# Kernel optimization log

Hardware: AMD Instinct MI355X
Metric: run time of the kernel (lower is better)

## Reference

```python
import jax, jax.numpy as jnp
import numpy as np

K = 5          # receptive field
N_IN = 4       # inputs per LUT node
DEPTH = 2      # tree depth -> layer widths [16, 4, 1]


def lut_nodes(s, lut):
    """Differentiable DWN LUT nodes.
    s:   [P, C, N, n] selected inputs in [0,1]
    lut: [C, N, 2**n] raw LUT weights (sigmoid applied -> entries in (0,1))
    out[p,c,m] = sum_a sigmoid(lut[c,m,a]) * prod_j s_j^{bit_j(a)} (1-s_j)^{1-bit_j(a)}
    Evaluated by contracting one address bit at a time (bit j=0 most significant).
    """
    n = s.shape[-1]
    C, N = lut.shape[0], lut.shape[1]
    t = jax.nn.sigmoid(lut).reshape((C, N) + (2,) * n)  # [C,N,2,...,2]
    for j in reversed(range(n)):
        xb = s[..., j].reshape(s.shape[:-1] + (1,) * j)  # [P,C,N,1*j]
        t = t[..., 0] * (1.0 - xb) + t[..., 1] * xb
    return t  # [P, C, N]


def extract_patches(x):
    """nn.Unfold(kernel=K, stride=1, pad=0): x [B,Cin,H,W] -> [B*P, Cin*K*K]."""
    B, Cin, H, W = x.shape
    Hp, Wp = H - K + 1, W - K + 1
    cols = jnp.stack([x[:, :, i:i + Hp, j:j + Wp]
                      for i in range(K) for j in range(K)], axis=2)  # [B,Cin,K*K,Hp,Wp]
    patches = cols.reshape(B, Cin * K * K, Hp * Wp)
    return patches.transpose(0, 2, 1).reshape(B * Hp * Wp, Cin * K * K), (B, Hp, Wp)


def setup_inputs() -> dict:
    key = jax.random.key(0)
    ks = jax.random.split(key, 7)
    C = 64
    return {
        "x": jax.random.uniform(ks[0], (32, 1, 32, 32), dtype=jnp.float32),
        "lut0": jax.random.normal(ks[1], (C, 16, 16), dtype=jnp.float32),
        "lut1": jax.random.normal(ks[2], (C, 4, 16), dtype=jnp.float32),
        "lut2": jax.random.normal(ks[3], (C, 1, 16), dtype=jnp.float32),
        "idx0": jax.random.randint(ks[4], (C, 16, N_IN), 0, 25, dtype=jnp.int32),
        "idx1": jax.random.randint(ks[5], (C, 4, N_IN), 0, 16, dtype=jnp.int32),
        "idx2": jax.random.randint(ks[6], (C, 1, N_IN), 0, 4, dtype=jnp.int32),
    }


def reference(x, lut0, lut1, lut2, idx0, idx1, idx2):
    patches, (B, Hp, Wp) = extract_patches(x)          # [P, 25]
    C = lut0.shape[0]
    # layer 0: gather raw patch features per channel/node
    s0 = patches[:, idx0]                              # [P, C, 16, 4]
    h0 = lut_nodes(s0, lut0)                           # [P, C, 16]
    # layer 1: per-channel gather from previous layer
    s1 = jnp.take_along_axis(h0[:, :, None, :], idx1[None], axis=-1)  # [P, C, 4, 4]
    h1 = lut_nodes(s1, lut1)                           # [P, C, 4]
    # layer 2 (root)
    s2 = jnp.take_along_axis(h1[:, :, None, :], idx2[None], axis=-1)  # [P, C, 1, 4]
    h2 = lut_nodes(s2, lut2)[..., 0]                   # [P, C]
    out = h2.reshape(B, Hp * Wp, C).transpose(0, 2, 1).reshape(B, C, Hp, Wp)
    return out
```

## Files before the change

kernel.cpp:

```cpp
#include <hip/hip_runtime.h>
#include <math.h>

#define KK 5
#define WPOUT 28
#define PPI 784
#define NCH 64
#define NPAIR 12544
#define THREADS 512
#define NNODE 21

typedef float f32x32 __attribute__((ext_vector_type(32)));
typedef float f32x16 __attribute__((ext_vector_type(16)));
typedef _Float16 h2  __attribute__((ext_vector_type(2)));

static __device__ __forceinline__ h2 u2h(unsigned u) { return __builtin_bit_cast(h2, u); }
static __device__ __forceinline__ unsigned h2u(h2 h) { return __builtin_bit_cast(unsigned, h); }
static __device__ __forceinline__ unsigned f2u(float f) { return __builtin_bit_cast(unsigned, f); }
static __device__ __forceinline__ float u2f(unsigned u) { return __builtin_bit_cast(float, u); }

static __device__ __forceinline__ unsigned packpair(float a, float b) {
    const auto pk = __builtin_amdgcn_cvt_pkrtz(a, b);
    return __builtin_bit_cast(unsigned, pk);
}

template <int ODD>
static __device__ __forceinline__ unsigned pkfma_splat(unsigned s, unsigned d, unsigned e) {
    unsigned r;
    if constexpr (ODD)
        asm("v_pk_fma_f16 %0, %1, %2, %3 op_sel:[0,1,1] op_sel_hi:[1,1,1]"
            : "=v"(r) : "v"(s), "v"(d), "v"(e));
    else
        asm("v_pk_fma_f16 %0, %1, %2, %3 op_sel:[0,0,0] op_sel_hi:[1,0,0]"
            : "=v"(r) : "v"(s), "v"(d), "v"(e));
    return r;
}

static __device__ __forceinline__ unsigned node_pair(uint4 E, uint4 D,
                                                     unsigned s0, unsigned s1,
                                                     unsigned s2, unsigned s3) {
    const unsigned Ea[4] = { E.x, E.y, E.z, E.w };
    const unsigned Da[4] = { D.x, D.y, D.z, D.w };
    unsigned v[8];
#pragma unroll
    for (int k = 0; k < 8; k += 2) {
        v[k]     = pkfma_splat<0>(s3, Da[k >> 1], Ea[k >> 1]);
        v[k + 1] = pkfma_splat<1>(s3, Da[k >> 1], Ea[k >> 1]);
    }
    const h2 s2h = u2h(s2), s1h = u2h(s1), s0h = u2h(s0);
    h2 w[4];
#pragma unroll
    for (int k = 0; k < 4; ++k) {
        const h2 ve = u2h(v[2 * k]), vo = u2h(v[2 * k + 1]);
        w[k] = s2h * (vo - ve) + ve;
    }
    const h2 u0 = s1h * (w[1] - w[0]) + w[0];
    const h2 u1 = s1h * (w[3] - w[2]) + w[2];
    return h2u(s0h * (u1 - u0) + u0);
}

__global__ __launch_bounds__(THREADS, 4)
void dwn_conv_lut_kernel(const float* __restrict__ x,
                         const float* __restrict__ lut0,
                         const float* __restrict__ lut1,
                         const float* __restrict__ lut2,
                         const int*   __restrict__ idx0,
                         const int*   __restrict__ idx1,
                         const int*   __restrict__ idx2,
                         float*       __restrict__ out)
{
    __shared__ __align__(16) _Float16 lut[NNODE][16];

    const int tid = threadIdx.x;
    const int c   = blockIdx.y;

    if (tid < NNODE * 8) {
        const int k = tid & 7, node = tid >> 3;
        const float* src;
        if (node < 16)      src = lut0 + (c * 16 + node) * 16;
        else if (node < 20) src = lut1 + (c * 4 + (node - 16)) * 16;
        else                src = lut2 + c * 16;
        const float a = src[2 * k], b = src[2 * k + 1];
        const float ea = 1.0f / (1.0f + __expf(-a));
        const float eb = 1.0f / (1.0f + __expf(-b));
        lut[node][k]     = (_Float16)ea;
        lut[node][k + 8] = (_Float16)(eb - ea);
    }

    __syncthreads();

    const int pi = blockIdx.x * THREADS + tid;
    if (pi >= NPAIR) return;
    const int p  = 2 * pi;
    const int b  = p / PPI;
    const int q  = p - b * PPI;
    const int i  = q / WPOUT;
    const int j  = q - i * WPOUT;

    const float* rp0 = x + b * 1024 + i * 32 + j;
    f32x32 pv;
#pragma unroll
    for (int di = 0; di < KK; ++di) {
        const float2* r2 = (const float2*)(rp0 + di * 32);
        const float2 w01 = r2[0], w23 = r2[1], w45 = r2[2];
        const float w[6] = { w01.x, w01.y, w23.x, w23.y, w45.x, w45.y };
#pragma unroll
        for (int dj = 0; dj < KK; ++dj) {
            pv[di * 5 + dj] = u2f(packpair(w[dj], w[dj + 1]));
        }
    }

    const int* id0 = idx0 + c * 64;
    f32x16 h0;
#pragma unroll
    for (int m = 0; m < 16; ++m) {
        const uint4* row = (const uint4*)&lut[m][0];
        const uint4 E = row[0], D = row[1];
        const int i0 = __builtin_amdgcn_readfirstlane(id0[m * 4 + 0]);
        const int i1 = __builtin_amdgcn_readfirstlane(id0[m * 4 + 1]);
        const int i2 = __builtin_amdgcn_readfirstlane(id0[m * 4 + 2]);
        const int i3 = __builtin_amdgcn_readfirstlane(id0[m * 4 + 3]);
        const unsigned r = node_pair(E, D, f2u(pv[i0]), f2u(pv[i1]), f2u(pv[i2]), f2u(pv[i3]));
        h0[m] = u2f(r);
    }

    const int* id1 = idx1 + c * 16;
    unsigned h1[4];
#pragma unroll
    for (int m = 0; m < 4; ++m) {
        const uint4* row = (const uint4*)&lut[16 + m][0];
        const uint4 E = row[0], D = row[1];
        const int i0 = __builtin_amdgcn_readfirstlane(id1[m * 4 + 0]);
        const int i1 = __builtin_amdgcn_readfirstlane(id1[m * 4 + 1]);
        const int i2 = __builtin_amdgcn_readfirstlane(id1[m * 4 + 2]);
        const int i3 = __builtin_amdgcn_readfirstlane(id1[m * 4 + 3]);
        h1[m] = node_pair(E, D, f2u(h0[i0]), f2u(h0[i1]), f2u(h0[i2]), f2u(h0[i3]));
    }

    const int* id2 = idx2 + c * 4;
    unsigned s[4];
#pragma unroll
    for (int jj = 0; jj < 4; ++jj) {
        const int ii = __builtin_amdgcn_readfirstlane(id2[jj]);
        s[jj] = (ii == 0) ? h1[0] : (ii == 1) ? h1[1] : (ii == 2) ? h1[2] : h1[3];
    }
    const uint4* row2 = (const uint4*)&lut[20][0];
    const h2 r = u2h(node_pair(row2[0], row2[1], s[0], s[1], s[2], s[3]));

    float2* o = (float2*)(out + (b * NCH + c) * PPI + q);
    *o = make_float2((float)r[0], (float)r[1]);
}

extern "C" void kernel_launch(void* const* d_in, const int* in_sizes, int n_in,
                              void* d_out, int out_size, void* d_ws, size_t ws_size,
                              hipStream_t stream) {
    const float* x    = (const float*)d_in[0];
    const float* lut0 = (const float*)d_in[1];
    const float* lut1 = (const float*)d_in[2];
    const float* lut2 = (const float*)d_in[3];
    const int*   idx0 = (const int*)d_in[4];
    const int*   idx1 = (const int*)d_in[5];
    const int*   idx2 = (const int*)d_in[6];
    float* out = (float*)d_out;

    dim3 grid((NPAIR + THREADS - 1) / THREADS, NCH);
    dim3 block(THREADS);
    dwn_conv_lut_kernel<<<grid, block, 0, stream>>>(x, lut0, lut1, lut2,
                                                    idx0, idx1, idx2, out);
}
```

Measured before the change: 23.54 us.

## Process two pixel pairs per thread, spilling second pair's state to LDS

Each thread now handles two pixel pairs, one in registers and one in a per-thread shared-memory scratch slice. The point is to amortize the LUT setup, index readfirstlane loads and LDS LUT reads over twice the work, and to raise ILP with two independent dependency chains. Block size shrinks to 128 and the grid halves. In exchange it adds LDS traffic (about 22 KB scratch per block) that may limit occupancy, and the per-thread slice stride may cause bank conflicts.

Measured after the change: 29.48 us. 1.25x slower.

```diff
diff --git a/kernel.cpp b/kernel.cpp
--- a/kernel.cpp
+++ b/kernel.cpp
@@ -6,8 +6,10 @@
 #define PPI 784
 #define NCH 64
 #define NPAIR 12544
-#define THREADS 512
+#define HPAIR 6272
+#define THREADS 128
 #define NNODE 21
+#define SLICE 43
 
 typedef float f32x32 __attribute__((ext_vector_type(32)));
 typedef float f32x16 __attribute__((ext_vector_type(16)));
@@ -58,6 +60,15 @@
     return h2u(s0h * (u1 - u0) + u0);
 }
 
+static __device__ __forceinline__ const float* pair_ptr(const float* x, int pi, int& b, int& q) {
+    const int p = 2 * pi;
+    b = p / PPI;
+    q = p - b * PPI;
+    const int i = q / WPOUT;
+    const int j = q - i * WPOUT;
+    return x + b * 1024 + i * 32 + j;
+}
+
 __global__ __launch_bounds__(THREADS, 4)
 void dwn_conv_lut_kernel(const float* __restrict__ x,
                          const float* __restrict__ lut0,
@@ -69,12 +80,13 @@
                          float*       __restrict__ out)
 {
     __shared__ __align__(16) _Float16 lut[NNODE][16];
+    __shared__ float scratch[THREADS * SLICE];
 
     const int tid = threadIdx.x;
     const int c   = blockIdx.y;
 
-    if (tid < NNODE * 8) {
-        const int k = tid & 7, node = tid >> 3;
+    for (int t = tid; t < NNODE * 8; t += THREADS) {
+        const int k = t & 7, node = t >> 3;
         const float* src;
         if (node < 16)      src = lut0 + (c * 16 + node) * 16;
         else if (node < 20) src = lut1 + (c * 4 + (node - 16)) * 16;
@@ -86,31 +98,34 @@
         lut[node][k + 8] = (_Float16)(eb - ea);
     }
 
-    __syncthreads();
+    const int piA = blockIdx.x * THREADS + tid;
+    const int piB = piA + HPAIR;
 
-    const int pi = blockIdx.x * THREADS + tid;
-    if (pi >= NPAIR) return;
-    const int p  = 2 * pi;
-    const int b  = p / PPI;
-    const int q  = p - b * PPI;
-    const int i  = q / WPOUT;
-    const int j  = q - i * WPOUT;
+    int bA, qA, bB, qB;
+    const float* rpA = pair_ptr(x, piA, bA, qA);
+    const float* rpB = pair_ptr(x, piB, bB, qB);
 
-    const float* rp0 = x + b * 1024 + i * 32 + j;
     f32x32 pv;
+    float* myB = &scratch[tid * SLICE];
 #pragma unroll
     for (int di = 0; di < KK; ++di) {
-        const float2* r2 = (const float2*)(rp0 + di * 32);
-        const float2 w01 = r2[0], w23 = r2[1], w45 = r2[2];
-        const float w[6] = { w01.x, w01.y, w23.x, w23.y, w45.x, w45.y };
+        const float2* a2 = (const float2*)(rpA + di * 32);
+        const float2 a01 = a2[0], a23 = a2[1], a45 = a2[2];
+        const float wa[6] = { a01.x, a01.y, a23.x, a23.y, a45.x, a45.y };
+        const float2* b2 = (const float2*)(rpB + di * 32);
+        const float2 b01 = b2[0], b23 = b2[1], b45 = b2[2];
+        const float wb[6] = { b01.x, b01.y, b23.x, b23.y, b45.x, b45.y };
 #pragma unroll
         for (int dj = 0; dj < KK; ++dj) {
-            pv[di * 5 + dj] = u2f(packpair(w[dj], w[dj + 1]));
+            pv[di * 5 + dj]  = u2f(packpair(wa[dj], wa[dj + 1]));
+            myB[di * 5 + dj] = u2f(packpair(wb[dj], wb[dj + 1]));
         }
     }
 
+    __syncthreads();
+
     const int* id0 = idx0 + c * 64;
-    f32x16 h0;
+    f32x16 h0A;
 #pragma unroll
     for (int m = 0; m < 16; ++m) {
         const uint4* row = (const uint4*)&lut[m][0];
@@ -119,12 +134,17 @@
         const int i1 = __builtin_amdgcn_readfirstlane(id0[m * 4 + 1]);
         const int i2 = __builtin_amdgcn_readfirstlane(id0[m * 4 + 2]);
         const int i3 = __builtin_amdgcn_readfirstlane(id0[m * 4 + 3]);
-        const unsigned r = node_pair(E, D, f2u(pv[i0]), f2u(pv[i1]), f2u(pv[i2]), f2u(pv[i3]));
-        h0[m] = u2f(r);
+        const unsigned b0 = f2u(myB[i0]);
+        const unsigned b1 = f2u(myB[i1]);
+        const unsigned b2 = f2u(myB[i2]);
+        const unsigned b3 = f2u(myB[i3]);
+        h0A[m] = u2f(node_pair(E, D, f2u(pv[i0]), f2u(pv[i1]), f2u(pv[i2]), f2u(pv[i3])));
+        const unsigned rB = node_pair(E, D, b0, b1, b2, b3);
+        myB[26 + m] = u2f(rB);
     }
 
     const int* id1 = idx1 + c * 16;
-    unsigned h1[4];
+    unsigned h1A[4], h1B[4];
 #pragma unroll
     for (int m = 0; m < 4; ++m) {
         const uint4* row = (const uint4*)&lut[16 + m][0];
@@ -133,21 +153,31 @@
         const int i1 = __builtin_amdgcn_readfirstlane(id1[m * 4 + 1]);
         const int i2 = __builtin_amdgcn_readfirstlane(id1[m * 4 + 2]);
         const int i3 = __builtin_amdgcn_readfirstlane(id1[m * 4 + 3]);
-        h1[m] = node_pair(E, D, f2u(h0[i0]), f2u(h0[i1]), f2u(h0[i2]), f2u(h0[i3]));
+        const unsigned b0 = f2u(myB[26 + i0]);
+        const unsigned b1 = f2u(myB[26 + i1]);
+        const unsigned b2 = f2u(myB[26 + i2]);
+        const unsigned b3 = f2u(myB[26 + i3]);
+        h1A[m] = node_pair(E, D, f2u(h0A[i0]), f2u(h0A[i1]), f2u(h0A[i2]), f2u(h0A[i3]));
+        h1B[m] = node_pair(E, D, b0, b1, b2, b3);
     }
 
     const int* id2 = idx2 + c * 4;
-    unsigned s[4];
+    unsigned sA[4], sB[4];
 #pragma unroll
     for (int jj = 0; jj < 4; ++jj) {
         const int ii = __builtin_amdgcn_readfirstlane(id2[jj]);
-        s[jj] = (ii == 0) ? h1[0] : (ii == 1) ? h1[1] : (ii == 2) ? h1[2] : h1[3];
+        sA[jj] = (ii == 0) ? h1A[0] : (ii == 1) ? h1A[1] : (ii == 2) ? h1A[2] : h1A[3];
+        sB[jj] = (ii == 0) ? h1B[0] : (ii == 1) ? h1B[1] : (ii == 2) ? h1B[2] : h1B[3];
     }
     const uint4* row2 = (const uint4*)&lut[20][0];
-    const h2 r = u2h(node_pair(row2[0], row2[1], s[0], s[1], s[2], s[3]));
+    const uint4 E2 = row2[0], D2 = row2[1];
+    const h2 rA = u2h(node_pair(E2, D2, sA[0], sA[1], sA[2], sA[3]));
+    const h2 rB = u2h(node_pair(E2, D2, sB[0], sB[1], sB[2], sB[3]));
 
-    float2* o = (float2*)(out + (b * NCH + c) * PPI + q);
-    *o = make_float2((float)r[0], (float)r[1]);
+    float2* oA = (float2*)(out + (bA * NCH + c) * PPI + qA);
+    *oA = make_float2((float)rA[0], (float)rA[1]);
+    float2* oB = (float2*)(out + (bB * NCH + c) * PPI + qB);
+    *oB = make_float2((float)rB[0], (float)rB[1]);
 }
 
 extern "C" void kernel_launch(void* const* d_in, const int* in_sizes, int n_in,
@@ -162,7 +192,7 @@
     const int*   idx2 = (const int*)d_in[6];
     float* out = (float*)d_out;
 
-    dim3 grid((NPAIR + THREADS - 1) / THREADS, NCH);
+    dim3 grid(HPAIR / THREADS, NCH);
     dim3 block(THREADS);
     dwn_conv_lut_kernel<<<grid, block, 0, stream>>>(x, lut0, lut1, lut2,
                                                     idx0, idx1, idx2, out);
```
